# Optimization experiments

Hardware: AMD Instinct MI355X
Metric: run time of the kernel (lower is better)

The kernel has to match this reference:

```python
import jax, jax.numpy as jnp
import numpy as np

N = 100000
E = 1600000


def setup_inputs() -> dict:
    key = jax.random.key(0)
    ks = jax.random.split(key, 8)
    x = jax.random.normal(ks[0], (N, 4), dtype=jnp.float32)
    edge_index = jax.random.randint(ks[1], (2, E), 0, N)
    # Glorot-ish scaled weights
    W1 = jax.random.normal(ks[2], (4, 64), dtype=jnp.float32) / np.sqrt(4.0)
    b1 = jnp.zeros((64,), dtype=jnp.float32)
    W2 = jax.random.normal(ks[3], (64, 32), dtype=jnp.float32) / np.sqrt(64.0)
    b2 = jnp.zeros((32,), dtype=jnp.float32)
    Wf = jax.random.normal(ks[4], (32, 32), dtype=jnp.float32) / np.sqrt(32.0)
    bf = jnp.zeros((32,), dtype=jnp.float32)
    return {"x": x, "edge_index": edge_index, "W1": W1, "b1": b1,
            "W2": W2, "b2": b2, "Wf": Wf, "bf": bf}


def _gcn_conv(x, W, b, src, dst, n):
    """PyG GCNConv: out = D^{-1/2}(A+I)D^{-1/2} (x @ W) + b, sum-aggregated at dst."""
    h = x @ W  # [n, out] -- linear before propagate, like PyG
    # degree over dst (self-loops already appended in src/dst)
    deg = jax.ops.segment_sum(jnp.ones_like(dst, dtype=h.dtype), dst, num_segments=n)
    dinv = jnp.where(deg > 0, jax.lax.rsqrt(jnp.maximum(deg, 1.0)), 0.0)
    norm = dinv[src] * dinv[dst]  # [E+n]
    msg = h[src] * norm[:, None]  # gather + scale
    out = jax.ops.segment_sum(msg, dst, num_segments=n)  # scatter-add
    return out + b


def reference(x, edge_index, W1, b1, W2, b2, Wf, bf):
    n = x.shape[0]
    loops = jnp.arange(n, dtype=edge_index.dtype)
    src = jnp.concatenate([edge_index[0], loops])
    dst = jnp.concatenate([edge_index[1], loops])
    h = jax.nn.relu(_gcn_conv(x, W1, b1, src, dst, n))
    h = jax.nn.relu(_gcn_conv(h, W2, b2, src, dst, n))
    return jax.nn.relu(h @ Wf + bf)
```

## Files before the change

kernel.cpp:

```cpp
#include <hip/hip_runtime.h>
#include <hip/hip_fp16.h>


#define STRIDE 64
#define BSHIFT 7
#define CH 8192
#define PBS 1024
#define PT (CH / PBS)

__global__ __launch_bounds__(PBS) void k_place(const int* __restrict__ src,
                                               const int* __restrict__ dst,
                                               int* __restrict__ gcur,
                                               int* __restrict__ ebuf,
                                               int NB, int CAP, int E) {
    __shared__ int stage[CH];
    __shared__ unsigned short stageb[CH];
    __shared__ int histA[1024];
    __shared__ int gbaseL[1024];
    __shared__ int wtot[16];
    const int tid = threadIdx.x;
    const int base = blockIdx.x * CH;
    const int blkcnt = min(CH, E - base);

    histA[tid] = 0;
    __syncthreads();

    int posr[PT];
    unsigned short bkr[PT];
    unsigned char lnr[PT];
#pragma unroll
    for (int k = 0; k < PT; ++k) {
        int e = base + tid + k * PBS;
        if (e < E) {
            int d = dst[e];
            int b = d >> BSHIFT;
            bkr[k] = (unsigned short)b;
            lnr[k] = (unsigned char)(d & 127);
            posr[k] = atomicAdd(&histA[b], 1);
        }
    }
    __syncthreads();

    {
        int lane = tid & 63, wid = tid >> 6;
        int v = histA[tid];
#pragma unroll
        for (int o = 1; o < 64; o <<= 1) {
            int t2 = __shfl_up(v, o, 64);
            if (lane >= o) v += t2;
        }
        if (lane == 63) wtot[wid] = v;
        __syncthreads();
        int wpre = 0;
        for (int ww = 0; ww < wid; ++ww) wpre += wtot[ww];
        histA[tid] = v + wpre;
    }
    __syncthreads();

    int* A = histA;

    if (tid < NB) {
        int st = tid ? A[tid - 1] : 0;
        int cnt = A[tid] - st;
        gbaseL[tid] = cnt ? atomicAdd(&gcur[tid], cnt) : 0;
    }
    __syncthreads();

#pragma unroll
    for (int k = 0; k < PT; ++k) {
        int e = base + tid + k * PBS;
        if (e < E) {
            int b = bkr[k];
            int st = b ? A[b - 1] : 0;
            int idx = st + posr[k];
            stage[idx] = src[e] | ((int)lnr[k] << 17);
            stageb[idx] = (unsigned short)b;
        }
    }
    __syncthreads();

    for (int j = tid; j < blkcnt; j += PBS) {
        int b = stageb[j];
        int st = b ? A[b - 1] : 0;
        int o = gbaseL[b] + (j - st);
        if (o < CAP) ebuf[(size_t)b * CAP + o] = stage[j];
    }
}

__global__ __launch_bounds__(512) void k_fillsorted2(const int* __restrict__ ebuf,
                                                     const int* __restrict__ gcur,
                                                     int* __restrict__ adjF,
                                                     int* __restrict__ deg,
                                                     float* __restrict__ dinv,
                                                     const float4* __restrict__ x,
                                                     float4* __restrict__ xd,
                                                     int CAP, int N) {
    __shared__ int adjL[128 * STRIDE];
    __shared__ int cnt[128];
    const int b = blockIdx.x, tid = threadIdx.x;
    if (tid < 128) cnt[tid] = 0;
    __syncthreads();

    int count = min(gcur[b], CAP);
    const int* eb = ebuf + (size_t)b * CAP;
    for (int j = tid; j < count; j += 512) {
        int v = eb[j];
        int ln = (v >> 17) & 127;
        int s = v & 0x1FFFF;
        int slot = atomicAdd(&cnt[ln], 1);
        if (slot < STRIDE) adjL[(ln << 6) | slot] = s;
    }
    __syncthreads();

    const size_t gbase = (size_t)b << 13;
    for (int j = tid; j < 128 * STRIDE; j += 512) {
        int rowc = cnt[j >> 6];
        if ((j & 63) < rowc) adjF[gbase + j] = adjL[j];
    }

    if (tid < 128) {
        int node = (b << BSHIFT) + tid;
        if (node < N) {
            int k = cnt[tid];
            deg[node] = k;
            float di = rsqrtf((float)(k + 1));
            dinv[node] = di;
            float4 xv = x[node];
            xv.x *= di; xv.y *= di; xv.z *= di; xv.w *= di;
            xd[node] = xv;
        }
    }
}

__global__ __launch_bounds__(512) void k_aggmlp(const int* __restrict__ deg,
                                                const int* __restrict__ adjF,
                                                const float4* __restrict__ xd,
                                                const float* __restrict__ dinv,
                                                const float* __restrict__ W1,
                                                const float* __restrict__ b1,
                                                const float* __restrict__ W2,
                                                signed char* __restrict__ Qq,
                                                float* __restrict__ Qs, int n) {
    __shared__ float4 aggL[64];
    const int tid = threadIdx.x;
    const int lane = tid & 31;
    const int sub = lane >> 3;
    const int sl  = lane & 7;
    const int nib = (tid >> 5) * 4 + sub;
    const int node = blockIdx.x * 64 + nib;
    bool valid = node < n;
    int nd = valid ? node : 0;
    int c = valid ? min(deg[nd], STRIDE) : 0;
    const int* row = adjF + ((size_t)nd << 6);

    float ax = 0.f, ay = 0.f, az = 0.f, aw = 0.f;
    int kk = sl;
    for (; kk + 8 < c; kk += 16) {
        int s0 = row[kk], s1 = row[kk + 8];
        float4 v0 = xd[s0];
        float4 v1 = xd[s1];
        ax += v0.x + v1.x; ay += v0.y + v1.y;
        az += v0.z + v1.z; aw += v0.w + v1.w;
    }
    if (kk < c) {
        float4 v = xd[row[kk]];
        ax += v.x; ay += v.y; az += v.z; aw += v.w;
    }
#pragma unroll
    for (int m = 4; m >= 1; m >>= 1) {
        ax += __shfl_xor(ax, m, 8);
        ay += __shfl_xor(ay, m, 8);
        az += __shfl_xor(az, m, 8);
        aw += __shfl_xor(aw, m, 8);
    }
    if (sl == 0) aggL[nib] = make_float4(ax, ay, az, aw);
    __syncthreads();

    if (tid < 64) {
        int i = blockIdx.x * 64 + tid;
        if (i < n) {
            float4 s = aggL[tid];
            float4 self = xd[i];
            float di = dinv[i];
            float bx = (s.x + self.x) * di, by = (s.y + self.y) * di;
            float bz = (s.z + self.z) * di, bw = (s.w + self.w) * di;

            float r[32];
#pragma unroll
            for (int cc = 0; cc < 32; ++cc) r[cc] = 0.0f;

#pragma unroll 8
            for (int j = 0; j < 64; ++j) {
                float h = fmaf(bx, W1[j], fmaf(by, W1[64 + j],
                          fmaf(bz, W1[128 + j], fmaf(bw, W1[192 + j], b1[j]))));
                h = fmaxf(h, 0.0f);
#pragma unroll
                for (int cc = 0; cc < 32; ++cc) r[cc] = fmaf(h, W2[j * 32 + cc], r[cc]);
            }

            float rm = 1e-12f;
#pragma unroll
            for (int cc = 0; cc < 32; ++cc) {
                r[cc] *= di;
                rm = fmaxf(rm, fabsf(r[cc]));
            }
            float inv = 127.0f / rm;
            unsigned pk[8];
#pragma unroll
            for (int g = 0; g < 8; ++g) {
                unsigned q0 = (unsigned)(__float2int_rn(r[4 * g + 0] * inv)) & 0xFFu;
                unsigned q1 = (unsigned)(__float2int_rn(r[4 * g + 1] * inv)) & 0xFFu;
                unsigned q2 = (unsigned)(__float2int_rn(r[4 * g + 2] * inv)) & 0xFFu;
                unsigned q3 = (unsigned)(__float2int_rn(r[4 * g + 3] * inv)) & 0xFFu;
                pk[g] = q0 | (q1 << 8) | (q2 << 16) | (q3 << 24);
            }
            uint4* qq = (uint4*)(Qq + ((size_t)i << 5));
            qq[0] = make_uint4(pk[0], pk[1], pk[2], pk[3]);
            qq[1] = make_uint4(pk[4], pk[5], pk[6], pk[7]);
            Qs[i] = rm * (1.0f / 127.0f);
        }
    }
}

__global__ void k_final(const int* __restrict__ deg, const int* __restrict__ adjF,
                        const float* __restrict__ dinv,
                        const signed char* __restrict__ Qq,
                        const float* __restrict__ Qs, const float* __restrict__ b2,
                        const float* __restrict__ Wf, const float* __restrict__ bf,
                        float* __restrict__ out, int n) {
    int node = blockIdx.x * (blockDim.x >> 5) + (threadIdx.x >> 5);
    int lane = threadIdx.x & 31;
    bool valid = node < n;
    int nd = valid ? node : 0;
    int c = valid ? min(deg[nd], STRIDE) : 0;
    const int* row = adjF + ((size_t)nd << 6);
    const int nb = lane >> 3;
    const int cw = lane & 7;

    float di   = dinv[nd];
    float bb2  = b2[lane];
    float bbf  = bf[lane];
    float qself = Qs[nd] * (float)Qq[((size_t)nd << 5) | lane];

    float a0 = 0.f, a1 = 0.f, a2 = 0.f, a3 = 0.f;
    for (int k = 0; k < c; k += 16) {
        int i0 = k + nb, i1 = k + 4 + nb, i2 = k + 8 + nb, i3 = k + 12 + nb;
        int s0 = row[min(i0, c - 1)];
        int s1 = row[min(i1, c - 1)];
        int s2 = row[min(i2, c - 1)];
        int s3 = row[min(i3, c - 1)];
        int w0 = ((const int*)(Qq + ((size_t)s0 << 5)))[cw];
        int w1 = ((const int*)(Qq + ((size_t)s1 << 5)))[cw];
        int w2 = ((const int*)(Qq + ((size_t)s2 << 5)))[cw];
        int w3 = ((const int*)(Qq + ((size_t)s3 << 5)))[cw];
        float sc0 = Qs[s0];
        float sc1 = Qs[s1];
        float sc2 = Qs[s2];
        float sc3 = Qs[s3];
        sc0 = (i0 < c) ? sc0 : 0.0f;
        sc1 = (i1 < c) ? sc1 : 0.0f;
        sc2 = (i2 < c) ? sc2 : 0.0f;
        sc3 = (i3 < c) ? sc3 : 0.0f;
        a0 = fmaf(sc0, (float)((signed char)(w0)), a0);
        a1 = fmaf(sc0, (float)((signed char)(w0 >> 8)), a1);
        a2 = fmaf(sc0, (float)((signed char)(w0 >> 16)), a2);
        a3 = fmaf(sc0, (float)(w0 >> 24), a3);
        a0 = fmaf(sc1, (float)((signed char)(w1)), a0);
        a1 = fmaf(sc1, (float)((signed char)(w1 >> 8)), a1);
        a2 = fmaf(sc1, (float)((signed char)(w1 >> 16)), a2);
        a3 = fmaf(sc1, (float)(w1 >> 24), a3);
        a0 = fmaf(sc2, (float)((signed char)(w2)), a0);
        a1 = fmaf(sc2, (float)((signed char)(w2 >> 8)), a1);
        a2 = fmaf(sc2, (float)((signed char)(w2 >> 16)), a2);
        a3 = fmaf(sc2, (float)(w2 >> 24), a3);
        a0 = fmaf(sc3, (float)((signed char)(w3)), a0);
        a1 = fmaf(sc3, (float)((signed char)(w3 >> 8)), a1);
        a2 = fmaf(sc3, (float)((signed char)(w3 >> 16)), a2);
        a3 = fmaf(sc3, (float)(w3 >> 24), a3);
    }

    a0 += __shfl_xor(a0, 8, 32);  a0 += __shfl_xor(a0, 16, 32);
    a1 += __shfl_xor(a1, 8, 32);  a1 += __shfl_xor(a1, 16, 32);
    a2 += __shfl_xor(a2, 8, 32);  a2 += __shfl_xor(a2, 16, 32);
    a3 += __shfl_xor(a3, 8, 32);  a3 += __shfl_xor(a3, 16, 32);

    int srcl = lane >> 2;
    float t0 = __shfl(a0, srcl, 32);
    float t1 = __shfl(a1, srcl, 32);
    float t2 = __shfl(a2, srcl, 32);
    float t3 = __shfl(a3, srcl, 32);
    int r2 = lane & 3;
    float accv = (r2 & 1) ? t1 : t0;
    float hi   = (r2 & 1) ? t3 : t2;
    accv = (r2 & 2) ? hi : accv;

    accv += qself;

    float h = fmaxf(fmaf(accv, di, bb2), 0.0f);
    float o = bbf;
#pragma unroll
    for (int cc = 0; cc < 32; ++cc) {
        o = fmaf(__shfl(h, cc, 32), Wf[cc * 32 + lane], o);
    }
    if (valid) out[((size_t)node << 5) | lane] = fmaxf(o, 0.0f);
}

static inline size_t align_up(size_t x, size_t a) { return (x + a - 1) & ~(a - 1); }

extern "C" void kernel_launch(void* const* d_in, const int* in_sizes, int n_in,
                              void* d_out, int out_size, void* d_ws, size_t ws_size,
                              hipStream_t stream) {
    const int N = in_sizes[0] / 4;
    const int E = in_sizes[1] / 2;

    const float* x  = (const float*)d_in[0];
    const int*   ei = (const int*)d_in[1];
    const int*   src = ei;
    const int*   dst = ei + E;
    const float* W1 = (const float*)d_in[2];
    const float* b1 = (const float*)d_in[3];
    const float* W2 = (const float*)d_in[4];
    const float* b2 = (const float*)d_in[5];
    const float* Wf = (const float*)d_in[6];
    const float* bf = (const float*)d_in[7];
    float* out = (float*)d_out;

    const int NB  = (N + 127) >> BSHIFT;
    const int CAP = ((E + NB - 1) / NB) * 5 / 4 + 64;

    char* w = (char*)d_ws;
    size_t off = 0;
    int*    gcur = (int*)(w + off);         off += align_up((size_t)NB * 4, 256);
    int*    deg  = (int*)(w + off);         off += align_up((size_t)N * 4, 256);
    float*  dinv = (float*)(w + off);       off += align_up((size_t)N * 4, 256);
    float*  xd   = (float*)(w + off);       off += align_up((size_t)N * 16, 256);
    int*    adjF = (int*)(w + off);         off += align_up((size_t)NB * 128 * STRIDE * 4, 256);
    signed char* Qq = (signed char*)(w + off); off += align_up((size_t)N * 32, 256);
    float*  Qs   = (float*)(w + off);       off += align_up((size_t)N * 4, 256);
    int*    ebuf = (int*)(w + off);         off += align_up((size_t)NB * CAP * 4, 256);

    const int B = 256;
    const int nplace = (E + CH - 1) / CH;

    hipMemsetAsync(gcur, 0, (size_t)NB * 4, stream);
    k_place<<<nplace, PBS, 0, stream>>>(src, dst, gcur, ebuf, NB, CAP, E);
    k_fillsorted2<<<NB, 512, 0, stream>>>(ebuf, gcur, adjF, deg, dinv,
                                          (const float4*)x, (float4*)xd, CAP, N);
    k_aggmlp<<<(N + 63) / 64, 512, 0, stream>>>(deg, adjF, (const float4*)xd,
                                                dinv, W1, b1, W2, Qq, Qs, N);
    k_final<<<((size_t)N * 32 + B - 1) / B, B, 0, stream>>>(deg, adjF, dinv, Qq, Qs,
                                                            b2, Wf, bf, out, N);
}
```

Before: 155.0 us.

## Zero-pad adjacency rows and prefetch first 32 neighbors unconditionally in aggregation kernels

The adjacency fill kernel now zeroes its shared rows and writes at least 32 entries per row, so unused slots hold a valid index (node 0). Both aggregation kernels issue the first 32 neighbor index loads and their feature gathers up front without waiting on the degree load, masking padded entries by multiplying by zero. This breaks the dependency chain deg -> loop bound -> row load -> gather and exposes more memory parallelism for the typical degree of about 16. The cost is extra writes of padded adjacency entries and wasted gathers for low-degree nodes.

```diff
diff --git a/kernel.cpp b/kernel.cpp
--- a/kernel.cpp
+++ b/kernel.cpp
@@ -98,6 +98,7 @@
     __shared__ int adjL[128 * STRIDE];
     __shared__ int cnt[128];
     const int b = blockIdx.x, tid = threadIdx.x;
+    for (int j = tid; j < 128 * STRIDE; j += 512) adjL[j] = 0;
     if (tid < 128) cnt[tid] = 0;
     __syncthreads();
 
@@ -115,7 +116,8 @@
     const size_t gbase = (size_t)b << 13;
     for (int j = tid; j < 128 * STRIDE; j += 512) {
         int rowc = cnt[j >> 6];
-        if ((j & 63) < rowc) adjF[gbase + j] = adjL[j];
+        int lim = (rowc <= 32) ? 32 : STRIDE;
+        if ((j & 63) < lim) adjF[gbase + j] = adjL[j];
     }
 
     if (tid < 128) {
@@ -150,19 +152,24 @@
     const int node = blockIdx.x * 64 + nib;
     bool valid = node < n;
     int nd = valid ? node : 0;
+    const int* row = adjF + ((size_t)nd << 6);
+
+    int r0 = row[sl], r1 = row[sl + 8], r2 = row[sl + 16], r3 = row[sl + 24];
     int c = valid ? min(deg[nd], STRIDE) : 0;
-    const int* row = adjF + ((size_t)nd << 6);
-
-    float ax = 0.f, ay = 0.f, az = 0.f, aw = 0.f;
-    int kk = sl;
-    for (; kk + 8 < c; kk += 16) {
-        int s0 = row[kk], s1 = row[kk + 8];
-        float4 v0 = xd[s0];
-        float4 v1 = xd[s1];
-        ax += v0.x + v1.x; ay += v0.y + v1.y;
-        az += v0.z + v1.z; aw += v0.w + v1.w;
-    }
-    if (kk < c) {
+    float4 v0 = xd[r0];
+    float4 v1 = xd[r1];
+    float4 v2 = xd[r2];
+    float4 v3 = xd[r3];
+    float m0 = (sl      < c) ? 1.0f : 0.0f;
+    float m1 = (sl + 8  < c) ? 1.0f : 0.0f;
+    float m2 = (sl + 16 < c) ? 1.0f : 0.0f;
+    float m3 = (sl + 24 < c) ? 1.0f : 0.0f;
+    float ax = fmaf(m0, v0.x, fmaf(m1, v1.x, fmaf(m2, v2.x, m3 * v3.x)));
+    float ay = fmaf(m0, v0.y, fmaf(m1, v1.y, fmaf(m2, v2.y, m3 * v3.y)));
+    float az = fmaf(m0, v0.z, fmaf(m1, v1.z, fmaf(m2, v2.z, m3 * v3.z)));
+    float aw = fmaf(m0, v0.w, fmaf(m1, v1.w, fmaf(m2, v2.w, m3 * v3.w)));
+
+    for (int kk = 32 + sl; kk < c; kk += 8) {
         float4 v = xd[row[kk]];
         ax += v.x; ay += v.y; az += v.z; aw += v.w;
     }
@@ -232,10 +239,15 @@
     int lane = threadIdx.x & 31;
     bool valid = node < n;
     int nd = valid ? node : 0;
-    int c = valid ? min(deg[nd], STRIDE) : 0;
     const int* row = adjF + ((size_t)nd << 6);
     const int nb = lane >> 3;
     const int cw = lane & 7;
+
+    int s[8];
+#pragma unroll
+    for (int g = 0; g < 8; ++g) s[g] = row[(g << 2) + nb];
+
+    int c = valid ? min(deg[nd], STRIDE) : 0;
 
     float di   = dinv[nd];
     float bb2  = b2[lane];
@@ -243,7 +255,18 @@
     float qself = Qs[nd] * (float)Qq[((size_t)nd << 5) | lane];
 
     float a0 = 0.f, a1 = 0.f, a2 = 0.f, a3 = 0.f;
-    for (int k = 0; k < c; k += 16) {
+#pragma unroll
+    for (int g = 0; g < 8; ++g) {
+        int wv = ((const int*)(Qq + ((size_t)s[g] << 5)))[cw];
+        float sc = Qs[s[g]];
+        sc = ((g << 2) + nb < c) ? sc : 0.0f;
+        a0 = fmaf(sc, (float)((signed char)(wv)), a0);
+        a1 = fmaf(sc, (float)((signed char)(wv >> 8)), a1);
+        a2 = fmaf(sc, (float)((signed char)(wv >> 16)), a2);
+        a3 = fmaf(sc, (float)(wv >> 24), a3);
+    }
+
+    for (int k = 32; k < c; k += 16) {
         int i0 = k + nb, i1 = k + 4 + nb, i2 = k + 8 + nb, i3 = k + 12 + nb;
         int s0 = row[min(i0, c - 1)];
         int s1 = row[min(i1, c - 1)];
@@ -253,14 +276,10 @@
         int w1 = ((const int*)(Qq + ((size_t)s1 << 5)))[cw];
         int w2 = ((const int*)(Qq + ((size_t)s2 << 5)))[cw];
         int w3 = ((const int*)(Qq + ((size_t)s3 << 5)))[cw];
-        float sc0 = Qs[s0];
-        float sc1 = Qs[s1];
-        float sc2 = Qs[s2];
-        float sc3 = Qs[s3];
-        sc0 = (i0 < c) ? sc0 : 0.0f;
-        sc1 = (i1 < c) ? sc1 : 0.0f;
-        sc2 = (i2 < c) ? sc2 : 0.0f;
-        sc3 = (i3 < c) ? sc3 : 0.0f;
+        float sc0 = Qs[s0]; sc0 = (i0 < c) ? sc0 : 0.0f;
+        float sc1 = Qs[s1]; sc1 = (i1 < c) ? sc1 : 0.0f;
+        float sc2 = Qs[s2]; sc2 = (i2 < c) ? sc2 : 0.0f;
+        float sc3 = Qs[s3]; sc3 = (i3 < c) ? sc3 : 0.0f;
         a0 = fmaf(sc0, (float)((signed char)(w0)), a0);
         a1 = fmaf(sc0, (float)((signed char)(w0 >> 8)), a1);
         a2 = fmaf(sc0, (float)((signed char)(w0 >> 16)), a2);
```

After: 149.9 us. 3.3% less time.
